# Kernel optimization log

Hardware: AMD Instinct MI355X
Metric: run time of the kernel (lower is better)

The kernel has to match this reference:

```python
import jax, jax.numpy as jnp
import numpy as np
import math

B, S, D = 16, 2048, 128

def setup_inputs() -> dict:
    key = jax.random.key(0)
    k1, k2, k3, k4 = jax.random.split(key, 4)
    query = jax.random.normal(k1, (B, S, D), dtype=jnp.float32)
    key_t = jax.random.normal(k2, (B, S, D), dtype=jnp.float32)
    value = jax.random.normal(k3, (B, S, D), dtype=jnp.float32)
    attn_mask = jax.random.randint(k4, (B, S, S), 0, 2).astype(bool)
    return {"query": query, "key": key_t, "value": value, "attn_mask": attn_mask}

def reference(query, key, value, attn_mask):
    # score = Q K^T / sqrt(d)  -> [B, Sq, Sk]
    scale = 1.0 / math.sqrt(query.shape[-1])
    score = jnp.einsum('bqd,bkd->bqk', query, key) * scale
    # faithful quirk: masked positions are replaced by the VALUE 1e-9 (not -inf)
    mask_score = jnp.where(attn_mask, jnp.float32(1e-9), score)
    # faithful quirk: softmax over dim=1 (the query axis), as in the torch source
    score_matrix = jax.nn.softmax(mask_score, axis=1)
    # output = softmax(scores) @ V  -> [B, Sq, D]
    output = jnp.einsum('bqk,bkd->bqd', score_matrix, value)
    return output
```

## Files before the change

### kernel.cpp

```cpp
#include <hip/hip_runtime.h>
#include <math.h>

#define NB 16
#define SS 2048
#define DQ 128
#define SCALE 0.08838834764831845f

typedef __bf16 bf16x8 __attribute__((ext_vector_type(8)));
typedef unsigned short ushort8_t __attribute__((ext_vector_type(8)));
typedef float floatx4 __attribute__((ext_vector_type(4)));

__device__ __forceinline__ unsigned short f2bf(float x) {
  unsigned int u = __float_as_uint(x);
  u += 0x7fffu + ((u >> 16) & 1u);
  return (unsigned short)(u >> 16);
}
union FragU { ushort8_t u; bf16x8 b; };
__device__ __forceinline__ bf16x8 ld_frag(const unsigned short* p) {
  FragU t; t.u = *(const ushort8_t*)p; return t.b;
}
__device__ __forceinline__ floatx4 mfma16(bf16x8 a, bf16x8 b, floatx4 c) {
  return __builtin_amdgcn_mfma_f32_16x16x32_bf16(a, b, c, 0, 0, 0);
}

__device__ __forceinline__ void bar_lds() {
  asm volatile("s_waitcnt lgkmcnt(0)\n\ts_barrier" ::: "memory");
}


__global__ void zero_accum(float* __restrict__ O) {
  float* p = O + (size_t)blockIdx.x * SS * DQ + 16 * DQ;
#pragma unroll
  for (int i = 0; i < 8; ++i) p[threadIdx.x + 256 * i] = 0.f;
}

template<int WRITE_E>
__global__ __launch_bounds__(256, 4) void pass1_colsum(
    const float* __restrict__ Q, const float* __restrict__ K,
    const int* __restrict__ M, float* __restrict__ O,
    unsigned short* __restrict__ E)
{
  const int k0  = blockIdx.x * 64;
  const int b   = blockIdx.y;
  const int qc  = blockIdx.z;
  const int tid = threadIdx.x;
  const int w = tid >> 6, lane = tid & 63, l15 = lane & 15, quad = lane >> 4;

  __shared__ unsigned short Kbf[64][136];
  __shared__ unsigned short Qbf[64][136];
  __shared__ float red[4][64];

  const float* Qb = Q + (size_t)b * SS * DQ;
  const float* Kb = K + (size_t)b * SS * DQ;
  const int*   Mb = M + (size_t)b * SS * SS;
  unsigned short* Eb = WRITE_E ? (E + (size_t)b * SS * SS) : nullptr;

  const int srow = tid >> 5;
  const int sc4  = (tid & 31) * 4;

#pragma unroll
  for (int r = 0; r < 8; ++r) {
    int row = srow + r * 8;
    float4 v = *(const float4*)(Kb + (size_t)(k0 + row) * DQ + sc4);
    *(ushort4*)&Kbf[row][sc4] = make_ushort4(f2bf(v.x), f2bf(v.y), f2bf(v.z), f2bf(v.w));
  }

  const int qlane = 16 * w + l15;

  float4 qreg[8];
  int4 mv_nxt[4];
  {
    const int q0 = qc * 512;
#pragma unroll
    for (int r = 0; r < 8; ++r)
      qreg[r] = *(const float4*)(Qb + (size_t)(q0 + srow + r * 8) * DQ + sc4);
#pragma unroll
    for (int i = 0; i < 4; ++i)
      mv_nxt[i] = *(const int4*)(Mb + (size_t)(q0 + qlane) * SS + k0 + 16 * i + quad * 4);
  }

  float colacc[16];
#pragma unroll
  for (int t = 0; t < 16; ++t) colacc[t] = 0.f;

  for (int qi = 0; qi < 8; ++qi) {
    bar_lds();
    int4 mv[4] = {mv_nxt[0], mv_nxt[1], mv_nxt[2], mv_nxt[3]};
#pragma unroll
    for (int r = 0; r < 8; ++r) {
      float4 v = qreg[r];
      *(ushort4*)&Qbf[srow + r * 8][sc4] =
          make_ushort4(f2bf(v.x), f2bf(v.y), f2bf(v.z), f2bf(v.w));
    }
    bar_lds();
    if (qi < 7) {
      const int qn = qc * 512 + (qi + 1) * 64;
#pragma unroll
      for (int r = 0; r < 8; ++r)
        qreg[r] = *(const float4*)(Qb + (size_t)(qn + srow + r * 8) * DQ + sc4);
#pragma unroll
      for (int i = 0; i < 4; ++i)
        mv_nxt[i] = *(const int4*)(Mb + (size_t)(qn + qlane) * SS + k0 + 16 * i + quad * 4);
    }

    floatx4 acc[4];
#pragma unroll
    for (int i = 0; i < 4; ++i) acc[i] = (floatx4){0.f, 0.f, 0.f, 0.f};
#pragma unroll
    for (int d0 = 0; d0 < DQ; d0 += 32) {
      bf16x8 bq = ld_frag(&Qbf[qlane][d0 + quad * 8]);
#pragma unroll
      for (int i = 0; i < 4; ++i) {
        bf16x8 ak = ld_frag(&Kbf[16 * i + l15][d0 + quad * 8]);
        acc[i] = mfma16(ak, bq, acc[i]);
      }
    }
    const int qrow = qc * 512 + qi * 64 + qlane;
#pragma unroll
    for (int i = 0; i < 4; ++i) {
      int mm[4] = {mv[i].x, mv[i].y, mv[i].z, mv[i].w};
      float ev[4];
#pragma unroll
      for (int r = 0; r < 4; ++r) {
        float s = mm[r] ? 1e-9f : acc[i][r] * SCALE;
        ev[r] = __expf(s);
        colacc[i * 4 + r] += ev[r];
      }
      if (WRITE_E) {
        *(ushort4*)(Eb + (size_t)qrow * SS + k0 + 16 * i + quad * 4) =
            make_ushort4(f2bf(ev[0]), f2bf(ev[1]), f2bf(ev[2]), f2bf(ev[3]));
      }
    }
  }

#pragma unroll
  for (int t = 0; t < 16; ++t) {
    colacc[t] += __shfl_xor(colacc[t], 1, 64);
    colacc[t] += __shfl_xor(colacc[t], 2, 64);
    colacc[t] += __shfl_xor(colacc[t], 4, 64);
    colacc[t] += __shfl_xor(colacc[t], 8, 64);
  }
  if (l15 == 0) {
#pragma unroll
    for (int i = 0; i < 4; ++i)
#pragma unroll
      for (int r = 0; r < 4; ++r)
        red[w][16 * i + quad * 4 + r] = colacc[i * 4 + r];
  }
  bar_lds();
  if (tid < 64) {
    float s = red[0][tid] + red[1][tid] + red[2][tid] + red[3][tid];
    atomicAdd(O + (size_t)b * SS * DQ + 16 * DQ + k0 + tid, s);
  }
}

__global__ void combine_linv(float* __restrict__ O) {
  const int b  = blockIdx.x;
  const int jb = blockIdx.y * 4;
  float* Ob = O + (size_t)b * SS * DQ;
#pragma unroll
  for (int it = 0; it < 8; ++it) {
    int k = threadIdx.x + 256 * it;
    float inv = 1.0f / Ob[16 * DQ + k];
#pragma unroll
    for (int j = 0; j < 4; ++j)
      Ob[(size_t)(64 * (jb + j)) * DQ + k] = inv;
  }
}

__global__ __launch_bounds__(256, 4) void pass2_pv(
    const float* __restrict__ V, const unsigned short* __restrict__ E,
    const float* __restrict__ O, float* __restrict__ P)
{
  const int b = blockIdx.z, q0 = blockIdx.x * 64, kh = blockIdx.y;
  const int kbase = kh * (SS / 2);
  const int tid = threadIdx.x;
  const int w = tid >> 6, lane = tid & 63, l15 = lane & 15, quad = lane >> 4;

  __shared__ unsigned short Wt[128][72];
  __shared__ float Li[SS / 2];

  const float* Vb = V + (size_t)b * SS * DQ;
  const unsigned short* Erow =
      E + (size_t)b * SS * SS + (size_t)(q0 + 16 * w + l15) * SS + kbase;

  const int sc4 = (tid & 31) * 4;
  const int vk2 = (tid >> 5) * 2;

  {
    const float* src = O + (size_t)b * SS * DQ + 16 * DQ + kbase;
    int idx = tid * 4;
    float4 c = *(const float4*)(src + idx);
    Li[idx + 0] = 1.0f / c.x;
    Li[idx + 1] = 1.0f / c.y;
    Li[idx + 2] = 1.0f / c.z;
    Li[idx + 3] = 1.0f / c.w;
  }

  floatx4 accO[8];
#pragma unroll
  for (int j = 0; j < 8; ++j) accO[j] = (floatx4){0.f, 0.f, 0.f, 0.f};

  float4 vreg[8];
  FragU ef_nxt[2];
  {
#pragma unroll
    for (int r = 0; r < 4; ++r) {
      int k2 = vk2 + r * 16;
      vreg[2 * r]     = *(const float4*)(Vb + (size_t)(kbase + k2)     * DQ + sc4);
      vreg[2 * r + 1] = *(const float4*)(Vb + (size_t)(kbase + k2 + 1) * DQ + sc4);
    }
#pragma unroll
    for (int c = 0; c < 2; ++c)
      ef_nxt[c].u = *(const ushort8_t*)(Erow + 32 * c + quad * 8);
  }

  for (int k0 = 0; k0 < SS / 2; k0 += 64) {
    bar_lds();
    FragU ef[2] = {ef_nxt[0], ef_nxt[1]};

#pragma unroll
    for (int r = 0; r < 4; ++r) {
      int k2 = vk2 + r * 16;
      float la = Li[k0 + k2], lb = Li[k0 + k2 + 1];
      float fa[4] = {vreg[2*r].x * la, vreg[2*r].y * la,
                     vreg[2*r].z * la, vreg[2*r].w * la};
      float fb[4] = {vreg[2*r+1].x * lb, vreg[2*r+1].y * lb,
                     vreg[2*r+1].z * lb, vreg[2*r+1].w * lb};
#pragma unroll
      for (int i = 0; i < 4; ++i) {
        int d  = sc4 + i;
        int kk = k2 ^ ((((unsigned)d >> 2) & 7) << 3);
        *(ushort2*)&Wt[d][kk] = make_ushort2(f2bf(fa[i]), f2bf(fb[i]));
      }
    }
    bar_lds();

    if (k0 + 64 < SS / 2) {
      const int kn = k0 + 64;
#pragma unroll
      for (int r = 0; r < 4; ++r) {
        int k2 = vk2 + r * 16;
        vreg[2 * r]     = *(const float4*)(Vb + (size_t)(kbase + kn + k2)     * DQ + sc4);
        vreg[2 * r + 1] = *(const float4*)(Vb + (size_t)(kbase + kn + k2 + 1) * DQ + sc4);
      }
#pragma unroll
      for (int c = 0; c < 2; ++c)
        ef_nxt[c].u = *(const ushort8_t*)(Erow + kn + 32 * c + quad * 8);
    }

#pragma unroll
    for (int c = 0; c < 2; ++c) {
      bf16x8 be = ef[c].b;
#pragma unroll
      for (int j = 0; j < 8; ++j) {
        int d  = 16 * j + l15;
        int kk = (32 * c + quad * 8) ^ ((((unsigned)d >> 2) & 7) << 3);
        bf16x8 aw = ld_frag(&Wt[d][kk]);
        accO[j] = mfma16(aw, be, accO[j]);
      }
    }
  }

#pragma unroll
  for (int j = 0; j < 8; ++j) {
    float* op = P + (((size_t)(kh * NB + b) * SS) + q0 + 16 * w + l15) * DQ
                  + 16 * j + quad * 4;
    *(float4*)op = make_float4(accO[j][0], accO[j][1], accO[j][2], accO[j][3]);
  }
}

__global__ void combine_O(const float* __restrict__ P, float* __restrict__ O) {
  const size_t boff = (size_t)blockIdx.x * SS * DQ + (size_t)blockIdx.y * 8192;
  const float* P0 = P + boff;
  const float* P1 = P + (size_t)NB * SS * DQ + boff;
  float* Ob = O + boff;
#pragma unroll
  for (int it = 0; it < 8; ++it) {
    int i = (threadIdx.x + 256 * it) * 4;
    float4 a = *(const float4*)(P0 + i);
    float4 c = *(const float4*)(P1 + i);
    *(float4*)(Ob + i) = make_float4(a.x + c.x, a.y + c.y, a.z + c.z, a.w + c.w);
  }
}

__global__ __launch_bounds__(256, 2) void pass2_out(
    const float* __restrict__ Q, const float* __restrict__ K,
    const float* __restrict__ V, const int* __restrict__ M,
    float* __restrict__ O)
{
  const int b = blockIdx.y, q0 = blockIdx.x * 64;
  const int tid = threadIdx.x;
  const int w = tid >> 6, lane = tid & 63, l15 = lane & 15, quad = lane >> 4;

  __shared__ unsigned short Kbf[64][136];
  __shared__ unsigned short Es[64][72];
  __shared__ unsigned short Wt[128][72];
  __shared__ float Li[SS];

  const float* Qb = Q + (size_t)b * SS * DQ;
  const float* Kb = K + (size_t)b * SS * DQ;
  const float* Vb = V + (size_t)b * SS * DQ;
  const int*   Mb = M + (size_t)b * SS * SS;

  const int srow = tid >> 5;
  const int sc4  = (tid & 31) * 4;

  {
    const float* src = O + ((size_t)b * SS + q0) * DQ;
#pragma unroll
    for (int r = 0; r < 2; ++r) {
      int idx = (tid + r * 256) * 4;
      *(float4*)&Li[idx] = *(const float4*)(src + idx);
    }
  }
  FragU qf[4];
  {
    const float* qrow = Qb + (size_t)(q0 + 16 * w + l15) * DQ;
#pragma unroll
    for (int i = 0; i < 4; ++i) {
      float4 a = *(const float4*)(qrow + 32 * i + quad * 8);
      float4 c = *(const float4*)(qrow + 32 * i + quad * 8 + 4);
      qf[i].u = (ushort8_t){f2bf(a.x), f2bf(a.y), f2bf(a.z), f2bf(a.w),
                            f2bf(c.x), f2bf(c.y), f2bf(c.z), f2bf(c.w)};
    }
  }

  floatx4 accO[8];
#pragma unroll
  for (int j = 0; j < 8; ++j) accO[j] = (floatx4){0.f, 0.f, 0.f, 0.f};

  const int* mrow = Mb + (size_t)(q0 + 16 * w + l15) * SS;

  float4 kreg[8], vreg[8];
  int4 mv_nxt[4];
  const int vk2 = (tid >> 5) * 2;
  {
#pragma unroll
    for (int r = 0; r < 8; ++r)
      kreg[r] = *(const float4*)(Kb + (size_t)(srow + r * 8) * DQ + sc4);
#pragma unroll
    for (int r = 0; r < 4; ++r) {
      int k2 = vk2 + r * 16;
      vreg[2 * r]     = *(const float4*)(Vb + (size_t)(k2)     * DQ + sc4);
      vreg[2 * r + 1] = *(const float4*)(Vb + (size_t)(k2 + 1) * DQ + sc4);
    }
#pragma unroll
    for (int j = 0; j < 4; ++j)
      mv_nxt[j] = *(const int4*)(mrow + 16 * j + quad * 4);
  }

  for (int k0 = 0; k0 < SS; k0 += 64) {
    bar_lds();
    int4 mv[4] = {mv_nxt[0], mv_nxt[1], mv_nxt[2], mv_nxt[3]};

#pragma unroll
    for (int r = 0; r < 8; ++r) {
      float4 v = kreg[r];
      *(ushort4*)&Kbf[srow + r * 8][sc4] =
          make_ushort4(f2bf(v.x), f2bf(v.y), f2bf(v.z), f2bf(v.w));
    }
#pragma unroll
    for (int r = 0; r < 4; ++r) {
      int k2 = vk2 + r * 16;
      float fa[4] = {vreg[2*r].x, vreg[2*r].y, vreg[2*r].z, vreg[2*r].w};
      float fb[4] = {vreg[2*r+1].x, vreg[2*r+1].y, vreg[2*r+1].z, vreg[2*r+1].w};
#pragma unroll
      for (int i = 0; i < 4; ++i) {
        int d  = sc4 + i;
        int kk = k2 ^ ((((unsigned)d >> 2) & 7) << 3);
        *(ushort2*)&Wt[d][kk] = make_ushort2(f2bf(fa[i]), f2bf(fb[i]));
      }
    }
    bar_lds();

    if (k0 + 64 < SS) {
      const int kn = k0 + 64;
#pragma unroll
      for (int r = 0; r < 8; ++r)
        kreg[r] = *(const float4*)(Kb + (size_t)(kn + srow + r * 8) * DQ + sc4);
#pragma unroll
      for (int r = 0; r < 4; ++r) {
        int k2 = vk2 + r * 16;
        vreg[2 * r]     = *(const float4*)(Vb + (size_t)(kn + k2)     * DQ + sc4);
        vreg[2 * r + 1] = *(const float4*)(Vb + (size_t)(kn + k2 + 1) * DQ + sc4);
      }
#pragma unroll
      for (int j = 0; j < 4; ++j)
        mv_nxt[j] = *(const int4*)(mrow + kn + 16 * j + quad * 4);
    }

    floatx4 acc[4];
#pragma unroll
    for (int j = 0; j < 4; ++j) acc[j] = (floatx4){0.f, 0.f, 0.f, 0.f};
#pragma unroll
    for (int i = 0; i < 4; ++i) {
      bf16x8 bq = qf[i].b;
#pragma unroll
      for (int j = 0; j < 4; ++j) {
        bf16x8 ak = ld_frag(&Kbf[16 * j + l15][32 * i + quad * 8]);
        acc[j] = mfma16(ak, bq, acc[j]);
      }
    }
#pragma unroll
    for (int j = 0; j < 4; ++j) {
      float4 liv = *(const float4*)&Li[k0 + 16 * j + quad * 4];
      float lv[4] = {liv.x, liv.y, liv.z, liv.w};
      int mm[4] = {mv[j].x, mv[j].y, mv[j].z, mv[j].w};
      unsigned short es[4];
#pragma unroll
      for (int r = 0; r < 4; ++r) {
        float s = mm[r] ? 1e-9f : acc[j][r] * SCALE;
        es[r] = f2bf(__expf(s) * lv[r]);
      }
      *(ushort4*)&Es[16 * w + l15][16 * j + quad * 4] =
          make_ushort4(es[0], es[1], es[2], es[3]);
    }
#pragma unroll
    for (int c = 0; c < 2; ++c) {
      bf16x8 be = ld_frag(&Es[16 * w + l15][32 * c + quad * 8]);
#pragma unroll
      for (int j = 0; j < 8; ++j) {
        int d  = 16 * j + l15;
        int kk = (32 * c + quad * 8) ^ ((((unsigned)d >> 2) & 7) << 3);
        bf16x8 aw = ld_frag(&Wt[d][kk]);
        accO[j] = mfma16(aw, be, accO[j]);
      }
    }
  }

#pragma unroll
  for (int j = 0; j < 8; ++j) {
    float* op = O + ((size_t)b * SS + q0 + 16 * w + l15) * DQ + 16 * j + quad * 4;
    *(float4*)op = make_float4(accO[j][0], accO[j][1], accO[j][2], accO[j][3]);
  }
}

extern "C" void kernel_launch(void* const* d_in, const int* in_sizes, int n_in,
                              void* d_out, int out_size, void* d_ws, size_t ws_size,
                              hipStream_t stream) {
  const float* Q = (const float*)d_in[0];
  const float* K = (const float*)d_in[1];
  const float* V = (const float*)d_in[2];
  const int*   M = (const int*)d_in[3];
  float* O = (float*)d_out;

  const size_t eneed = (size_t)NB * SS * SS * sizeof(unsigned short);
  const size_t pneed = eneed + (size_t)2 * NB * SS * DQ * sizeof(float);

  zero_accum<<<dim3(NB), 256, 0, stream>>>(O);
  if (d_ws != nullptr && ws_size >= pneed) {
    unsigned short* E = (unsigned short*)d_ws;
    float* P = (float*)((char*)d_ws + eneed);
    pass1_colsum<1><<<dim3(32, NB, 4), 256, 0, stream>>>(Q, K, M, O, E);
    pass2_pv<<<dim3(32, 2, NB), 256, 0, stream>>>(V, E, O, P);
    combine_O<<<dim3(NB, 32), 256, 0, stream>>>(P, O);
  } else {
    pass1_colsum<0><<<dim3(32, NB, 4), 256, 0, stream>>>(Q, K, M, O, nullptr);
    combine_linv<<<dim3(NB, 8), 256, 0, stream>>>(O);
    pass2_out<<<dim3(32, NB), 256, 0, stream>>>(Q, K, V, M, O);
  }
}
```

Before: 524.1 us.

## Precompute scaled bf16 transposed V and split PV pass four ways

Adds a make_vt kernel that scales V by the inverse column sums once, converts it to bf16 and writes it transposed to workspace. pass2_pv then loads its MFMA A-fragments straight from global memory, with no LDS staging or per-block rescaling and no barriers. The key dimension is split four ways instead of two to get more blocks, and combine_O now sums four partial outputs. In exchange it needs more workspace, an extra kernel launch and larger partial-result traffic. Fragment loads from global are strided by SS per row and rely on cache hits.

```diff
diff --git a/kernel.cpp b/kernel.cpp
--- a/kernel.cpp
+++ b/kernel.cpp
@@ -4,6 +4,7 @@
 #define NB 16
 #define SS 2048
 #define DQ 128
+#define KHN 4
 #define SCALE 0.08838834764831845f
 
 typedef __bf16 bf16x8 __attribute__((ext_vector_type(8)));
@@ -154,6 +155,112 @@
   }
 }
 
+__global__ __launch_bounds__(256, 4) void make_vt(
+    const float* __restrict__ V, const float* __restrict__ O,
+    unsigned short* __restrict__ Vt)
+{
+  const int b  = blockIdx.x;
+  const int ks = blockIdx.y * 128;
+  const int tid = threadIdx.x;
+
+  __shared__ unsigned short T[128][136];
+
+  const float* Vb = V + ((size_t)b * SS + ks) * DQ;
+  const float* Cs = O + (size_t)b * SS * DQ + 16 * DQ + ks;
+
+  const int kr  = tid >> 5;
+  const int sc4 = (tid & 31) * 4;
+
+#pragma unroll
+  for (int r = 0; r < 16; ++r) {
+    int k = kr + r * 8;
+    float inv = 1.0f / Cs[k];
+    float4 v = *(const float4*)(Vb + (size_t)k * DQ + sc4);
+    float f[4] = {v.x * inv, v.y * inv, v.z * inv, v.w * inv};
+#pragma unroll
+    for (int i = 0; i < 4; ++i) {
+      int d = sc4 + i;
+      T[d][k ^ (((d >> 2) & 15) << 3)] = f2bf(f[i]);
+    }
+  }
+  bar_lds();
+
+  unsigned short* Vo = Vt + (size_t)b * DQ * SS + ks;
+#pragma unroll
+  for (int it = 0; it < 8; ++it) {
+    int idx = tid + 256 * it;
+    int d = idx >> 4, seg = (idx & 15) * 8;
+    int kk = seg ^ (((d >> 2) & 15) << 3);
+    *(ushort8_t*)(Vo + (size_t)d * SS + seg) = *(const ushort8_t*)&T[d][kk];
+  }
+}
+
+__global__ __launch_bounds__(256, 4) void pass2_pv(
+    const unsigned short* __restrict__ Vt, const unsigned short* __restrict__ E,
+    float* __restrict__ P)
+{
+  const int b = blockIdx.z, q0 = blockIdx.x * 64, kh = blockIdx.y;
+  const int kbase = kh * (SS / KHN);
+  const int tid = threadIdx.x;
+  const int w = tid >> 6, lane = tid & 63, l15 = lane & 15, quad = lane >> 4;
+
+  const unsigned short* Erow =
+      E + (size_t)b * SS * SS + (size_t)(q0 + 16 * w + l15) * SS + kbase;
+  const unsigned short* vrow =
+      Vt + (size_t)b * DQ * SS + (size_t)l15 * SS + kbase + quad * 8;
+
+  floatx4 accO[8];
+#pragma unroll
+  for (int j = 0; j < 8; ++j) accO[j] = (floatx4){0.f, 0.f, 0.f, 0.f};
+
+  FragU ef_nxt[2];
+  ef_nxt[0].u = *(const ushort8_t*)(Erow + quad * 8);
+  ef_nxt[1].u = *(const ushort8_t*)(Erow + 32 + quad * 8);
+
+  for (int k0 = 0; k0 < SS / KHN; k0 += 64) {
+    FragU ef0 = ef_nxt[0], ef1 = ef_nxt[1];
+    if (k0 + 64 < SS / KHN) {
+      ef_nxt[0].u = *(const ushort8_t*)(Erow + k0 + 64 + quad * 8);
+      ef_nxt[1].u = *(const ushort8_t*)(Erow + k0 + 96 + quad * 8);
+    }
+#pragma unroll
+    for (int c = 0; c < 2; ++c) {
+      bf16x8 be = (c == 0) ? ef0.b : ef1.b;
+#pragma unroll
+      for (int j = 0; j < 8; ++j) {
+        bf16x8 aw = ld_frag(vrow + (size_t)j * 16 * SS + k0 + 32 * c);
+        accO[j] = mfma16(aw, be, accO[j]);
+      }
+    }
+  }
+
+#pragma unroll
+  for (int j = 0; j < 8; ++j) {
+    float* op = P + (((size_t)(kh * NB + b) * SS) + q0 + 16 * w + l15) * DQ
+                  + 16 * j + quad * 4;
+    *(float4*)op = make_float4(accO[j][0], accO[j][1], accO[j][2], accO[j][3]);
+  }
+}
+
+__global__ void combine_O(const float* __restrict__ P, float* __restrict__ O) {
+  const size_t boff = (size_t)blockIdx.x * SS * DQ + (size_t)blockIdx.y * 8192;
+  const size_t str = (size_t)NB * SS * DQ;
+  const float* P0 = P + boff;
+  float* Ob = O + boff;
+#pragma unroll
+  for (int it = 0; it < 8; ++it) {
+    int i = (threadIdx.x + 256 * it) * 4;
+    float4 a = *(const float4*)(P0 + i);
+    float4 c = *(const float4*)(P0 + str + i);
+    float4 d = *(const float4*)(P0 + 2 * str + i);
+    float4 e = *(const float4*)(P0 + 3 * str + i);
+    *(float4*)(Ob + i) = make_float4(a.x + c.x + d.x + e.x,
+                                     a.y + c.y + d.y + e.y,
+                                     a.z + c.z + d.z + e.z,
+                                     a.w + c.w + d.w + e.w);
+  }
+}
+
 __global__ void combine_linv(float* __restrict__ O) {
   const int b  = blockIdx.x;
   const int jb = blockIdx.y * 4;
@@ -165,122 +272,6 @@
 #pragma unroll
     for (int j = 0; j < 4; ++j)
       Ob[(size_t)(64 * (jb + j)) * DQ + k] = inv;
-  }
-}
-
-__global__ __launch_bounds__(256, 4) void pass2_pv(
-    const float* __restrict__ V, const unsigned short* __restrict__ E,
-    const float* __restrict__ O, float* __restrict__ P)
-{
-  const int b = blockIdx.z, q0 = blockIdx.x * 64, kh = blockIdx.y;
-  const int kbase = kh * (SS / 2);
-  const int tid = threadIdx.x;
-  const int w = tid >> 6, lane = tid & 63, l15 = lane & 15, quad = lane >> 4;
-
-  __shared__ unsigned short Wt[128][72];
-  __shared__ float Li[SS / 2];
-
-  const float* Vb = V + (size_t)b * SS * DQ;
-  const unsigned short* Erow =
-      E + (size_t)b * SS * SS + (size_t)(q0 + 16 * w + l15) * SS + kbase;
-
-  const int sc4 = (tid & 31) * 4;
-  const int vk2 = (tid >> 5) * 2;
-
-  {
-    const float* src = O + (size_t)b * SS * DQ + 16 * DQ + kbase;
-    int idx = tid * 4;
-    float4 c = *(const float4*)(src + idx);
-    Li[idx + 0] = 1.0f / c.x;
-    Li[idx + 1] = 1.0f / c.y;
-    Li[idx + 2] = 1.0f / c.z;
-    Li[idx + 3] = 1.0f / c.w;
-  }
-
-  floatx4 accO[8];
-#pragma unroll
-  for (int j = 0; j < 8; ++j) accO[j] = (floatx4){0.f, 0.f, 0.f, 0.f};
-
-  float4 vreg[8];
-  FragU ef_nxt[2];
-  {
-#pragma unroll
-    for (int r = 0; r < 4; ++r) {
-      int k2 = vk2 + r * 16;
-      vreg[2 * r]     = *(const float4*)(Vb + (size_t)(kbase + k2)     * DQ + sc4);
-      vreg[2 * r + 1] = *(const float4*)(Vb + (size_t)(kbase + k2 + 1) * DQ + sc4);
-    }
-#pragma unroll
-    for (int c = 0; c < 2; ++c)
-      ef_nxt[c].u = *(const ushort8_t*)(Erow + 32 * c + quad * 8);
-  }
-
-  for (int k0 = 0; k0 < SS / 2; k0 += 64) {
-    bar_lds();
-    FragU ef[2] = {ef_nxt[0], ef_nxt[1]};
-
-#pragma unroll
-    for (int r = 0; r < 4; ++r) {
-      int k2 = vk2 + r * 16;
-      float la = Li[k0 + k2], lb = Li[k0 + k2 + 1];
-      float fa[4] = {vreg[2*r].x * la, vreg[2*r].y * la,
-                     vreg[2*r].z * la, vreg[2*r].w * la};
-      float fb[4] = {vreg[2*r+1].x * lb, vreg[2*r+1].y * lb,
-                     vreg[2*r+1].z * lb, vreg[2*r+1].w * lb};
-#pragma unroll
-      for (int i = 0; i < 4; ++i) {
-        int d  = sc4 + i;
-        int kk = k2 ^ ((((unsigned)d >> 2) & 7) << 3);
-        *(ushort2*)&Wt[d][kk] = make_ushort2(f2bf(fa[i]), f2bf(fb[i]));
-      }
-    }
-    bar_lds();
-
-    if (k0 + 64 < SS / 2) {
-      const int kn = k0 + 64;
-#pragma unroll
-      for (int r = 0; r < 4; ++r) {
-        int k2 = vk2 + r * 16;
-        vreg[2 * r]     = *(const float4*)(Vb + (size_t)(kbase + kn + k2)     * DQ + sc4);
-        vreg[2 * r + 1] = *(const float4*)(Vb + (size_t)(kbase + kn + k2 + 1) * DQ + sc4);
-      }
-#pragma unroll
-      for (int c = 0; c < 2; ++c)
-        ef_nxt[c].u = *(const ushort8_t*)(Erow + kn + 32 * c + quad * 8);
-    }
-
-#pragma unroll
-    for (int c = 0; c < 2; ++c) {
-      bf16x8 be = ef[c].b;
-#pragma unroll
-      for (int j = 0; j < 8; ++j) {
-        int d  = 16 * j + l15;
-        int kk = (32 * c + quad * 8) ^ ((((unsigned)d >> 2) & 7) << 3);
-        bf16x8 aw = ld_frag(&Wt[d][kk]);
-        accO[j] = mfma16(aw, be, accO[j]);
-      }
-    }
-  }
-
-#pragma unroll
-  for (int j = 0; j < 8; ++j) {
-    float* op = P + (((size_t)(kh * NB + b) * SS) + q0 + 16 * w + l15) * DQ
-                  + 16 * j + quad * 4;
-    *(float4*)op = make_float4(accO[j][0], accO[j][1], accO[j][2], accO[j][3]);
-  }
-}
-
-__global__ void combine_O(const float* __restrict__ P, float* __restrict__ O) {
-  const size_t boff = (size_t)blockIdx.x * SS * DQ + (size_t)blockIdx.y * 8192;
-  const float* P0 = P + boff;
-  const float* P1 = P + (size_t)NB * SS * DQ + boff;
-  float* Ob = O + boff;
-#pragma unroll
-  for (int it = 0; it < 8; ++it) {
-    int i = (threadIdx.x + 256 * it) * 4;
-    float4 a = *(const float4*)(P0 + i);
-    float4 c = *(const float4*)(P1 + i);
-    *(float4*)(Ob + i) = make_float4(a.x + c.x, a.y + c.y, a.z + c.z, a.w + c.w);
   }
 }
 
@@ -445,15 +436,19 @@
   const int*   M = (const int*)d_in[3];
   float* O = (float*)d_out;
 
-  const size_t eneed = (size_t)NB * SS * SS * sizeof(unsigned short);
-  const size_t pneed = eneed + (size_t)2 * NB * SS * DQ * sizeof(float);
+  const size_t esz = (size_t)NB * SS * SS * sizeof(unsigned short);
+  const size_t psz = (size_t)KHN * NB * SS * DQ * sizeof(float);
+  const size_t vsz = (size_t)NB * DQ * SS * sizeof(unsigned short);
+  const size_t need = esz + psz + vsz;
 
   zero_accum<<<dim3(NB), 256, 0, stream>>>(O);
-  if (d_ws != nullptr && ws_size >= pneed) {
+  if (d_ws != nullptr && ws_size >= need) {
     unsigned short* E = (unsigned short*)d_ws;
-    float* P = (float*)((char*)d_ws + eneed);
+    float* P = (float*)((char*)d_ws + esz);
+    unsigned short* Vt = (unsigned short*)((char*)d_ws + esz + psz);
     pass1_colsum<1><<<dim3(32, NB, 4), 256, 0, stream>>>(Q, K, M, O, E);
-    pass2_pv<<<dim3(32, 2, NB), 256, 0, stream>>>(V, E, O, P);
+    make_vt<<<dim3(NB, 16), 256, 0, stream>>>(V, O, Vt);
+    pass2_pv<<<dim3(32, KHN, NB), 256, 0, stream>>>(Vt, E, P);
     combine_O<<<dim3(NB, 32), 256, 0, stream>>>(P, O);
   } else {
     pass1_colsum<0><<<dim3(32, NB, 4), 256, 0, stream>>>(Q, K, M, O, nullptr);
```

After: 606.8 us. +15.8%, slower.
